# Kernel optimization log

Measured on AMD Instinct MI355X. Metric: run time of the kernel, lower is better.

## Reference

```python
import jax, jax.numpy as jnp
import numpy as np

C = 128      # hidden_dim
H = 8        # nheads
HD = C // H  # head_dim = 16
SCALE = HD ** (-0.5)
Q = 100      # num_queries
T = 5        # t
DM = 512     # d_model
AD = 128     # audio feature dim
EPS = 1e-5


def _ln(x, g, b):
    m = jnp.mean(x, -1, keepdims=True)
    v = jnp.mean((x - m) ** 2, -1, keepdims=True)
    return (x - m) / jnp.sqrt(v + EPS) * g + b


def _heads(x):
    bt, L, c = x.shape
    return x.reshape(bt, L, H, c // H).transpose(0, 2, 1, 3)  # (bt,H,L,hd)


def _unheads(x):
    bt, h, L, d = x.shape
    return x.transpose(0, 2, 1, 3).reshape(bt, L, h * d)


def _attn(q, k, v):
    a = jax.nn.softmax(jnp.einsum('bhqd,bhkd->bhqk', q, k) * SCALE, axis=-1)
    return jnp.einsum('bhqk,bhkd->bhqd', a, v)


def setup_inputs() -> dict:
    key = jax.random.key(0)
    ks = iter(jax.random.split(key, 40))
    def nrm(shape, s=0.02):
        return jax.random.normal(next(ks), shape, dtype=jnp.float32) * s
    bt, hw = 40, 1024
    return {
        'audio_feat': jax.random.normal(next(ks), (bt, hw, AD), dtype=jnp.float32),
        'vis_feat': jax.random.normal(next(ks), (bt, hw, DM), dtype=jnp.float32),
        'iq_emb': nrm((Q, C), 0.1),
        'w_iqp': nrm((C, 2 * C)), 'b_iqp': jnp.zeros((2 * C,), jnp.float32),
        'w_afp': nrm((AD, 2 * C)), 'b_afp': jnp.zeros((2 * C,), jnp.float32),
        'w_vfp': nrm((DM, 2 * C)), 'b_vfp': jnp.zeros((2 * C,), jnp.float32),
        'g_an': jnp.ones((2 * C,), jnp.float32), 'be_an': jnp.zeros((2 * C,), jnp.float32),
        'g_vn': jnp.ones((2 * C,), jnp.float32), 'be_vn': jnp.zeros((2 * C,), jnp.float32),
        'w_aqp': nrm((C, 2 * C)), 'b_aqp': jnp.zeros((2 * C,), jnp.float32),
        'w_vqp': nrm((C, 2 * C)), 'b_vqp': jnp.zeros((2 * C,), jnp.float32),
        'w_aq': nrm((AD, C)), 'b_aq': jnp.zeros((C,), jnp.float32),
        'w_vq': nrm((DM, C)), 'b_vq': jnp.zeros((C,), jnp.float32),
        'w_in': nrm((C, 3 * C)), 'b_in': jnp.zeros((3 * C,), jnp.float32),
        'w_o': nrm((C, C)), 'b_o': jnp.zeros((C,), jnp.float32),
        'w_ao': nrm((C, DM)), 'b_ao': jnp.zeros((DM,), jnp.float32),
        'w_vo': nrm((C, DM)), 'b_vo': jnp.zeros((DM,), jnp.float32),
    }


def reference(audio_feat, vis_feat, iq_emb, w_iqp, b_iqp, w_afp, b_afp,
              w_vfp, b_vfp, g_an, be_an, g_vn, be_vn, w_aqp, b_aqp,
              w_vqp, b_vqp, w_aq, b_aq, w_vq, b_vq, w_in, b_in, w_o, b_o,
              w_ao, b_ao, w_vo, b_vo):
    bt, hw, _ = vis_feat.shape
    bs = bt // T

    # intermediate query projection -> audio / vis query sets
    aq0, vq0 = jnp.split(iq_emb @ w_iqp + b_iqp, 2, axis=-1)  # (Q, C) each
    aqh = _heads(jnp.broadcast_to(aq0, (bt, Q, C)))
    vqh = _heads(jnp.broadcast_to(vq0, (bt, Q, C)))

    # feature K/V (LayerNorm over 2C then chunk)
    a_ki, a_vi = jnp.split(_ln(audio_feat @ w_afp + b_afp, g_an, be_an), 2, axis=-1)
    v_ki, v_vi = jnp.split(_ln(vis_feat @ w_vfp + b_vfp, g_vn, be_vn), 2, axis=-1)

    # cross-attn: queries attend to features, with residual on queries
    aiq = _unheads(_attn(aqh, _heads(a_ki), _heads(a_vi)) + aqh)  # (bt,Q,C)
    viq = _unheads(_attn(vqh, _heads(v_ki), _heads(v_vi)) + vqh)

    # self-attn over concatenated queries across time (per sample)
    queries = jnp.concatenate([aiq, viq], axis=1).reshape(bs, T * 2 * Q, C)
    qkv = queries @ w_in + b_in
    q, k, v = jnp.split(qkv, 3, axis=-1)
    sa = _unheads(_attn(_heads(q), _heads(k), _heads(v))) @ w_o + b_o
    queries = sa.reshape(bt, 2 * Q, C)
    aiq2, viq2 = queries[:, :Q], queries[:, Q:]

    # fused queries become K/V for the features
    a_kf, a_vf = jnp.split(aiq2 @ w_aqp + b_aqp, 2, axis=-1)
    v_kf, v_vf = jnp.split(viq2 @ w_vqp + b_vqp, 2, axis=-1)
    _a = _heads(audio_feat @ w_aq + b_aq)
    _v = _heads(vis_feat @ w_vq + b_vq)

    a_att = _unheads(_attn(_a, _heads(v_kf), _heads(v_vf)))  # (bt,hw,C)
    audio_out = (a_att + audio_feat) @ w_ao + b_ao            # (bt,hw,DM)

    v_att = _unheads(_attn(_v, _heads(a_kf), _heads(a_vf)))   # (bt,hw,C)
    vis_out = v_att @ w_vo + b_vo + vis_feat                  # (bt,hw,DM)

    return (audio_out, vis_out, aiq2)
```

## Files before the change

### kernel.cpp

```cpp
#include <hip/hip_runtime.h>

#define EPSF 1e-5f
#define SCALEF 0.25f

typedef __attribute__((ext_vector_type(8))) __bf16 bf16x8;
typedef __attribute__((ext_vector_type(8))) unsigned short sh8;
typedef __attribute__((ext_vector_type(4))) float f32x4;

__device__ __forceinline__ unsigned short f2bf(float f) {
  unsigned u = __float_as_uint(f);
  return (unsigned short)((u + 0x7FFFu + ((u >> 16) & 1u)) >> 16);
}
__device__ __forceinline__ unsigned pk2(float lo, float hi) {
  return (unsigned)f2bf(lo) | ((unsigned)f2bf(hi) << 16);
}
__device__ __forceinline__ float bf2f(unsigned short u) {
  return __uint_as_float((unsigned)u << 16);
}

__device__ __forceinline__ void gll16(const void* g, void* l) {
  __builtin_amdgcn_global_load_lds((const __attribute__((address_space(1))) void*)g,
                                   (__attribute__((address_space(3))) void*)l,
                                   16, 0, 0);
}

template <int K, int BN, int EPI, bool POST, bool AHEAD, bool OBF, bool PBF, bool AF32>
__global__ __launch_bounds__(BN * 2) void mfma_gemm(
    const unsigned short* __restrict__ A, const unsigned short* __restrict__ Wt,
    const float* __restrict__ bias, const float* __restrict__ gg,
    const float* __restrict__ be, const float* __restrict__ post,
    float* __restrict__ C, int M, int Ntot, int ATPB, int CTPB, size_t CPS,
    float* __restrict__ aiq2, const float* __restrict__ Af32,
    unsigned short* __restrict__ Aside) {
  constexpr int NW = BN / 32;
  constexpr int NCW = BN / 64;
  __shared__ __align__(16) unsigned short As[128 * 32];
  __shared__ __align__(16) unsigned short Bs[BN * 32];
  __shared__ float2 part[128][4];
  const int tid = threadIdx.x;
  const int wid = tid >> 6, lane = tid & 63;
  const int wr = wid / NCW, wc = wid % NCW;
  const int m0t = blockIdx.x * 128, n0t = blockIdx.y * BN;
  const int ir = lane >> 2, sl = lane & 3;
  const int sg = lane >> 4, li = lane & 15;
  f32x4 acc[4][4];
#pragma unroll
  for (int i = 0; i < 4; i++)
#pragma unroll
    for (int j = 0; j < 4; j++) acc[i][j] = (f32x4){0.f, 0.f, 0.f, 0.f};
  constexpr int nIss = 8 + BN / 16;

  for (int k0 = 0; k0 < K; k0 += 32) {
    __syncthreads();
    if constexpr (AF32) {
      int r = tid >> 2, slp = tid & 3;
      int sp = slp ^ ((r >> 1) & 3);
      const float4* src = (const float4*)(Af32 + (size_t)(m0t + r) * K + k0 + sp * 8);
      float4 aa = src[0], bb = src[1];
      uint4 w;
      w.x = pk2(aa.x, aa.y); w.y = pk2(aa.z, aa.w);
      w.z = pk2(bb.x, bb.y); w.w = pk2(bb.z, bb.w);
      *(uint4*)&As[r * 32 + slp * 8] = w;
      *(uint4*)(Aside + (size_t)(m0t + r) * K + k0 + sp * 8) = w;
      for (int is = 8 + wid; is < nIss; is += NW) {
        int r2 = (is - 8) * 16 + ir;
        int sp2 = sl ^ ((r2 >> 1) & 3);
        gll16(Wt + (size_t)(n0t + r2) * K + k0 + sp2 * 8, (void*)&Bs[(is - 8) * 512]);
      }
    } else {
      for (int is = wid; is < nIss; is += NW) {
        if (is < 8) {
          int r = is * 16 + ir;
          int sp = sl ^ ((r >> 1) & 3);
          const unsigned short* gsrc;
          if (AHEAD) {
            int rg = m0t + r;
            if (rg >= M) rg = M - 1;
            int b = rg / ATPB, tok = rg - b * ATPB;
            int e = k0 + sp * 8;
            gsrc = A + ((((size_t)b * 8 + (e >> 4)) * ATPB + tok) << 4) + (e & 15);
          } else {
            gsrc = A + (size_t)(m0t + r) * K + k0 + sp * 8;
          }
          gll16(gsrc, (void*)&As[is * 512]);
        } else {
          int r = (is - 8) * 16 + ir;
          int sp = sl ^ ((r >> 1) & 3);
          gll16(Wt + (size_t)(n0t + r) * K + k0 + sp * 8, (void*)&Bs[(is - 8) * 512]);
        }
      }
    }
    __syncthreads();
    bf16x8 af[4], bfr[4];
#pragma unroll
    for (int mi = 0; mi < 4; mi++) {
      int m = wr * 64 + mi * 16 + li;
      sh8 t = *(const sh8*)&As[m * 32 + ((sg ^ ((m >> 1) & 3)) << 3)];
      af[mi] = __builtin_bit_cast(bf16x8, t);
    }
#pragma unroll
    for (int ni = 0; ni < 4; ni++) {
      int n = wc * 64 + ni * 16 + li;
      sh8 t = *(const sh8*)&Bs[n * 32 + ((sg ^ ((n >> 1) & 3)) << 3)];
      bfr[ni] = __builtin_bit_cast(bf16x8, t);
    }
#pragma unroll
    for (int mi = 0; mi < 4; mi++)
#pragma unroll
      for (int ni = 0; ni < 4; ni++)
        acc[mi][ni] = __builtin_amdgcn_mfma_f32_16x16x32_bf16(af[mi], bfr[ni],
                                                              acc[mi][ni], 0, 0, 0);
  }

  float bv[4];
#pragma unroll
  for (int ni = 0; ni < 4; ni++) bv[ni] = bias[n0t + wc * 64 + ni * 16 + li];

  if constexpr (EPI == 1) {
#pragma unroll
    for (int mi = 0; mi < 4; mi++)
#pragma unroll
      for (int ni = 0; ni < 4; ni++)
#pragma unroll
        for (int r = 0; r < 4; r++) acc[mi][ni][r] += bv[ni];
#pragma unroll
    for (int mi = 0; mi < 4; mi++)
#pragma unroll
      for (int r = 0; r < 4; r++) {
        float s = acc[mi][0][r] + acc[mi][1][r] + acc[mi][2][r] + acc[mi][3][r];
        float q2 = acc[mi][0][r] * acc[mi][0][r] + acc[mi][1][r] * acc[mi][1][r] +
                   acc[mi][2][r] * acc[mi][2][r] + acc[mi][3][r] * acc[mi][3][r];
#pragma unroll
        for (int off = 1; off < 16; off <<= 1) {
          s += __shfl_xor(s, off);
          q2 += __shfl_xor(q2, off);
        }
        if (li == 0) part[wr * 64 + mi * 16 + sg * 4 + r][wc] = make_float2(s, q2);
      }
    __syncthreads();
    float gv[4], bev[4];
#pragma unroll
    for (int ni = 0; ni < 4; ni++) {
      int col = wc * 64 + ni * 16 + li;
      gv[ni] = gg[col];
      bev[ni] = be[col];
    }
#pragma unroll
    for (int mi = 0; mi < 4; mi++)
#pragma unroll
      for (int r = 0; r < 4; r++) {
        int mrow = wr * 64 + mi * 16 + sg * 4 + r;
        float2 p0 = part[mrow][0], p1 = part[mrow][1], p2 = part[mrow][2], p3 = part[mrow][3];
        float S = p0.x + p1.x + p2.x + p3.x;
        float Qq = p0.y + p1.y + p2.y + p3.y;
        float mean = S * (1.f / 256.f);
        float var = Qq * (1.f / 256.f) - mean * mean;
        float rstd = rsqrtf(var + EPSF);
        int mg = m0t + mrow;
        int b = mg / CTPB, tok = mg - b * CTPB;
#pragma unroll
        for (int ni = 0; ni < 4; ni++) {
          int col = wc * 64 + ni * 16 + li;
          float val = (acc[mi][ni][r] - mean) * rstd * gv[ni] + bev[ni];
          int half = col >> 7, h = (col >> 4) & 7, d = col & 15;
          size_t idx = ((((size_t)b * 8 + h) * CTPB + tok) << 4) + d;
          if (OBF) {
            unsigned short* dst = (unsigned short*)C + (half ? CPS : 0);
            dst[idx] = f2bf(val);
          } else {
            float* dst = half ? (C + CPS) : C;
            dst[idx] = val;
          }
        }
      }
  } else if constexpr (EPI == 2) {
#pragma unroll
    for (int mi = 0; mi < 4; mi++)
#pragma unroll
      for (int r = 0; r < 4; r++) {
        int mg = m0t + wr * 64 + mi * 16 + sg * 4 + r;
        if (mg < M) {
          int b = mg / CTPB, tok = mg - b * CTPB;
#pragma unroll
          for (int ni = 0; ni < 4; ni++) {
            int col = n0t + wc * 64 + ni * 16 + li;
            float v = acc[mi][ni][r] + bv[ni];
            int pt = col >> 7, h = (col >> 4) & 7, d = col & 15;
            size_t idx = ((((size_t)b * 8 + h) * CTPB + tok) << 4) + d;
            if (OBF)
              ((unsigned short*)C + (size_t)pt * CPS)[idx] = f2bf(v);
            else
              (C + (size_t)pt * CPS)[idx] = v;
          }
        }
      }
  } else {
#pragma unroll
    for (int mi = 0; mi < 4; mi++)
#pragma unroll
      for (int r = 0; r < 4; r++) {
        int mrow = m0t + wr * 64 + mi * 16 + sg * 4 + r;
        if (mrow < M) {
#pragma unroll
          for (int ni = 0; ni < 4; ni++) {
            int col = n0t + wc * 64 + ni * 16 + li;
            float v = acc[mi][ni][r] + bv[ni];
            if (POST) {
              if (PBF)
                v += bf2f(((const unsigned short*)post)[(size_t)mrow * Ntot + col]);
              else
                v += post[(size_t)mrow * Ntot + col];
            }
            C[(size_t)mrow * Ntot + col] = v;
            if (aiq2) {
              int fb = mrow / 200, wi2 = mrow % 200;
              if (wi2 < 100) aiq2[((size_t)fb * 100 + wi2) * Ntot + col] = v;
            }
          }
        }
      }
  }
}

__global__ __launch_bounds__(512) void mattn1(
    const float* __restrict__ aqvq,
    const unsigned short* __restrict__ akn, const unsigned short* __restrict__ avn,
    const unsigned short* __restrict__ vkn, const unsigned short* __restrict__ vvn,
    unsigned short* __restrict__ op) {
  __shared__ __align__(16) unsigned short Klds[64][24];
  __shared__ __align__(16) unsigned short VTlds[16][72];
  __shared__ __align__(16) unsigned short Plds[8][16][72];
  const int tid = threadIdx.x, wid = tid >> 6, lane = tid & 63;
  const int li = lane & 15, gr = lane >> 4;
  const int z = blockIdx.z, h = blockIdx.y;
  const int mod = z >= 40 ? 1 : 0;
  const int b = z - mod * 40;
  const int bh = b * 8 + h;
  const int qi = wid * 16 + li;
  const bool qact = qi < 100;
  const int qic = qact ? qi : 99;
  const float* qrow = aqvq + mod * 128 + (size_t)qic * 256 + h * 16;
  const unsigned short* kp = mod ? vkn : akn;
  const unsigned short* vp = mod ? vvn : avn;

  sh8 z8 = (sh8)0;
  bf16x8 qf = __builtin_bit_cast(bf16x8, z8);
  if (gr < 2) {
    const float4* q4 = (const float4*)(qrow + gr * 8);
    float4 qa = q4[0], qb = q4[1];
    sh8 tt;
    tt[0] = f2bf(qa.x); tt[1] = f2bf(qa.y); tt[2] = f2bf(qa.z); tt[3] = f2bf(qa.w);
    tt[4] = f2bf(qb.x); tt[5] = f2bf(qb.y); tt[6] = f2bf(qb.z); tt[7] = f2bf(qb.w);
    qf = __builtin_bit_cast(bf16x8, tt);
  }

  float mrun = -3e38f, lrun = 0.f;
  f32x4 acc = (f32x4){0.f, 0.f, 0.f, 0.f};
  const f32x4 zero4 = (f32x4){0.f, 0.f, 0.f, 0.f};
  const unsigned* Ku = (const unsigned*)(kp + (size_t)bh * 1024 * 16);
  const unsigned* Vu = (const unsigned*)(vp + (size_t)bh * 1024 * 16);
  const int skey = tid >> 3, sdb = tid & 7;

  unsigned kw = Ku[(size_t)skey * 8 + sdb];
  unsigned vw = Vu[(size_t)skey * 8 + sdb];
  for (int kb = 0; kb < 1024; kb += 64) {
    __syncthreads();
    *(unsigned*)&Klds[skey][sdb * 2] = kw;
    VTlds[sdb * 2 + 0][skey] = (unsigned short)(vw & 0xffff);
    VTlds[sdb * 2 + 1][skey] = (unsigned short)(vw >> 16);
    if (kb + 64 < 1024) {
      kw = Ku[(size_t)(kb + 64 + skey) * 8 + sdb];
      vw = Vu[(size_t)(kb + 64 + skey) * 8 + sdb];
    }
    __syncthreads();
    f32x4 st[4];
#pragma unroll
    for (int t = 0; t < 4; t++) {
      sh8 kk = *(const sh8*)&Klds[t * 16 + li][(gr & 1) * 8];
      st[t] = __builtin_amdgcn_mfma_f32_16x16x32_bf16(
          __builtin_bit_cast(bf16x8, kk), qf, zero4, 0, 0, 0);
    }
    float sv[4][4];
#pragma unroll
    for (int t = 0; t < 4; t++)
#pragma unroll
      for (int r = 0; r < 4; r++) sv[t][r] = st[t][r] * SCALEF;
    float bm = sv[0][0];
#pragma unroll
    for (int t = 0; t < 4; t++)
#pragma unroll
      for (int r = 0; r < 4; r++) bm = fmaxf(bm, sv[t][r]);
    bm = fmaxf(bm, __shfl_xor(bm, 16));
    bm = fmaxf(bm, __shfl_xor(bm, 32));
    float mnew = fmaxf(mrun, bm);
    float cf = __expf(mrun - mnew);
    mrun = mnew;
    lrun *= cf;
    acc[0] *= cf; acc[1] *= cf; acc[2] *= cf; acc[3] *= cf;
    float ls = 0.f;
    unsigned pw[4][2];
#pragma unroll
    for (int t = 0; t < 4; t++) {
      float p0 = __expf(sv[t][0] - mnew), p1 = __expf(sv[t][1] - mnew);
      float p2 = __expf(sv[t][2] - mnew), p3 = __expf(sv[t][3] - mnew);
      ls += (p0 + p1) + (p2 + p3);
      pw[t][0] = pk2(p0, p1);
      pw[t][1] = pk2(p2, p3);
    }
    ls += __shfl_xor(ls, 16);
    ls += __shfl_xor(ls, 32);
    lrun += ls;
#pragma unroll
    for (int t = 0; t < 4; t++)
      *(uint2*)&Plds[wid][li][t * 16 + gr * 4] = make_uint2(pw[t][0], pw[t][1]);
#pragma unroll
    for (int hh = 0; hh < 2; hh++) {
      sh8 vt = *(const sh8*)&VTlds[li][hh * 32 + gr * 8];
      sh8 pt = *(const sh8*)&Plds[wid][li][hh * 32 + gr * 8];
      acc = __builtin_amdgcn_mfma_f32_16x16x32_bf16(
          __builtin_bit_cast(bf16x8, vt), __builtin_bit_cast(bf16x8, pt), acc, 0, 0, 0);
    }
  }
  float inv = 1.f / lrun;
  float o[4];
#pragma unroll
  for (int r = 0; r < 4; r++) o[r] = acc[r] * inv;
  const float4* q4 = (const float4*)(qrow + gr * 4);
  float4 qv = q4[0];
  o[0] += qv.x; o[1] += qv.y; o[2] += qv.z; o[3] += qv.w;
  if (qact) {
    int obh = (b / 5) * 8 + h;
    int otok = (b % 5) * 200 + mod * 100 + qi;
    *(uint2*)(op + (((size_t)obh * 1000 + otok) << 4) + gr * 4) =
        make_uint2(pk2(o[0], o[1]), pk2(o[2], o[3]));
  }
}

template <int MODE>
__global__ __launch_bounds__(512) void mattn8(
    const unsigned short* __restrict__ q0s, const unsigned short* __restrict__ q1s,
    size_t qsb, size_t qsh, int qsr,
    const unsigned short* __restrict__ k0s, const unsigned short* __restrict__ v0s,
    const unsigned short* __restrict__ k1s, const unsigned short* __restrict__ v1s,
    int nk, int nq, unsigned short* __restrict__ o0s, unsigned short* __restrict__ o1s,
    int OTPB, const unsigned short* __restrict__ residbf) {
  __shared__ __align__(16) unsigned short Klds[64][24];
  __shared__ __align__(16) unsigned short VTlds[16][72];
  __shared__ __align__(16) unsigned short Plds[8][16][72];
  const int tid = threadIdx.x, wid = tid >> 6, lane = tid & 63;
  const int li = lane & 15, gr = lane >> 4;
  const int z = blockIdx.z, h = blockIdx.y;
  int mod = 0, b = z;
  const unsigned short *qp = q0s, *kp = k0s, *vp = v0s;
  unsigned short* op = o0s;
  if (MODE == 2) {
    mod = z >= 40 ? 1 : 0;
    b = z - mod * 40;
    if (mod) { qp = q1s; kp = k1s; vp = v1s; op = o1s; }
  }
  const int bh = b * 8 + h;
  const int qi = blockIdx.x * 128 + wid * 16 + li;
  const bool qact = qi < nq;
  const int qic = qact ? qi : nq - 1;
  const unsigned short* qrow = qp + b * qsb + h * qsh + (size_t)qic * qsr;

  sh8 z8 = (sh8)0;
  bf16x8 qf = __builtin_bit_cast(bf16x8, z8);
  if (gr < 2) qf = __builtin_bit_cast(bf16x8, *(const sh8*)(qrow + gr * 8));

  float mrun = -3e38f, lrun = 0.f;
  f32x4 acc = (f32x4){0.f, 0.f, 0.f, 0.f};
  const f32x4 zero4 = (f32x4){0.f, 0.f, 0.f, 0.f};
  const unsigned* Ku = (const unsigned*)(kp + (size_t)bh * nk * 16);
  const unsigned* Vu = (const unsigned*)(vp + (size_t)bh * nk * 16);
  const int skey = tid >> 3, sdb = tid & 7;

  unsigned kw = (skey < nk) ? Ku[(size_t)skey * 8 + sdb] : 0u;
  unsigned vw = (skey < nk) ? Vu[(size_t)skey * 8 + sdb] : 0u;
  for (int kb = 0; kb < nk; kb += 64) {
    __syncthreads();
    *(unsigned*)&Klds[skey][sdb * 2] = kw;
    VTlds[sdb * 2 + 0][skey] = (unsigned short)(vw & 0xffff);
    VTlds[sdb * 2 + 1][skey] = (unsigned short)(vw >> 16);
    if (kb + 64 < nk) {
      int gk = kb + 64 + skey;
      kw = (gk < nk) ? Ku[(size_t)gk * 8 + sdb] : 0u;
      vw = (gk < nk) ? Vu[(size_t)gk * 8 + sdb] : 0u;
    }
    __syncthreads();
    f32x4 st[4];
#pragma unroll
    for (int t = 0; t < 4; t++) {
      sh8 kk = *(const sh8*)&Klds[t * 16 + li][(gr & 1) * 8];
      st[t] = __builtin_amdgcn_mfma_f32_16x16x32_bf16(
          __builtin_bit_cast(bf16x8, kk), qf, zero4, 0, 0, 0);
    }
    float sv[4][4];
#pragma unroll
    for (int t = 0; t < 4; t++)
#pragma unroll
      for (int r = 0; r < 4; r++) sv[t][r] = st[t][r] * SCALEF;
    if (kb + 64 > nk) {
#pragma unroll
      for (int t = 0; t < 4; t++) {
        int kbase = kb + t * 16 + gr * 4;
#pragma unroll
        for (int r = 0; r < 4; r++)
          if (kbase + r >= nk) sv[t][r] = -1e30f;
      }
    }
    float bm = sv[0][0];
#pragma unroll
    for (int t = 0; t < 4; t++)
#pragma unroll
      for (int r = 0; r < 4; r++) bm = fmaxf(bm, sv[t][r]);
    bm = fmaxf(bm, __shfl_xor(bm, 16));
    bm = fmaxf(bm, __shfl_xor(bm, 32));
    float mnew = fmaxf(mrun, bm);
    float cf = __expf(mrun - mnew);
    mrun = mnew;
    lrun *= cf;
    acc[0] *= cf; acc[1] *= cf; acc[2] *= cf; acc[3] *= cf;
    float ls = 0.f;
    unsigned pw[4][2];
#pragma unroll
    for (int t = 0; t < 4; t++) {
      float p0 = __expf(sv[t][0] - mnew), p1 = __expf(sv[t][1] - mnew);
      float p2 = __expf(sv[t][2] - mnew), p3 = __expf(sv[t][3] - mnew);
      ls += (p0 + p1) + (p2 + p3);
      pw[t][0] = pk2(p0, p1);
      pw[t][1] = pk2(p2, p3);
    }
    ls += __shfl_xor(ls, 16);
    ls += __shfl_xor(ls, 32);
    lrun += ls;
#pragma unroll
    for (int t = 0; t < 4; t++)
      *(uint2*)&Plds[wid][li][t * 16 + gr * 4] = make_uint2(pw[t][0], pw[t][1]);
#pragma unroll
    for (int hh = 0; hh < 2; hh++) {
      sh8 vt = *(const sh8*)&VTlds[li][hh * 32 + gr * 8];
      sh8 pt = *(const sh8*)&Plds[wid][li][hh * 32 + gr * 8];
      acc = __builtin_amdgcn_mfma_f32_16x16x32_bf16(
          __builtin_bit_cast(bf16x8, vt), __builtin_bit_cast(bf16x8, pt), acc, 0, 0, 0);
    }
  }
  float inv = 1.f / lrun;
  float o[4];
#pragma unroll
  for (int r = 0; r < 4; r++) o[r] = acc[r] * inv;
  if (MODE == 2 && mod == 0 && residbf) {
    uint2 rv = *(const uint2*)(residbf + ((size_t)b * 1024 + qic) * 128 + h * 16 + gr * 4);
    o[0] += bf2f((unsigned short)(rv.x & 0xffff));
    o[1] += bf2f((unsigned short)(rv.x >> 16));
    o[2] += bf2f((unsigned short)(rv.y & 0xffff));
    o[3] += bf2f((unsigned short)(rv.y >> 16));
  }
  if (qact) {
    *(uint2*)(op + (((size_t)bh * OTPB + qi) << 4) + gr * 4) =
        make_uint2(pk2(o[0], o[1]), pk2(o[2], o[3]));
  }
}

__global__ __launch_bounds__(256) void prep_kernel(
    const float* __restrict__ iq, const float* __restrict__ w_iqp,
    const float* __restrict__ b_iqp,
    const float* __restrict__ w_afp, const float* __restrict__ w_vfp,
    const float* __restrict__ w_aq, const float* __restrict__ w_vq,
    const float* __restrict__ w_in, const float* __restrict__ w_o,
    const float* __restrict__ w_ao, const float* __restrict__ w_vo,
    unsigned short* __restrict__ WT, float* __restrict__ aqvq) {
  __shared__ float row[128];
  const int g = blockIdx.x, tid = threadIdx.x;
  if (g < 1728) {
    int lg = g;
    int K, N;
    const float* W;
    unsigned dst;
    if (lg < 128)       { K = 128; N = 256; W = w_afp; dst = 0; }
    else if (lg < 640)  { K = 512; N = 256; W = w_vfp; dst = 32768;  lg -= 128; }
    else if (lg < 704)  { K = 128; N = 128; W = w_aq;  dst = 163840; lg -= 640; }
    else if (lg < 960)  { K = 512; N = 128; W = w_vq;  dst = 180224; lg -= 704; }
    else if (lg < 1152) { K = 128; N = 384; W = w_in;  dst = 245760; lg -= 960; }
    else if (lg < 1216) { K = 128; N = 128; W = w_o;   dst = 294912; lg -= 1152; }
    else if (lg < 1472) { K = 128; N = 512; W = w_ao;  dst = 311296; lg -= 1216; }
    else                { K = 128; N = 512; W = w_vo;  dst = 376832; lg -= 1472; }
    int idx = lg * 256 + tid;
    if (idx < K * N) {
      int k = idx / N, n = idx - k * N;
      WT[dst + (size_t)n * K + k] = f2bf(W[idx]);
    }
  } else {
    int r = g - 1728;
    if (tid < 128) row[tid] = iq[r * 128 + tid];
    __syncthreads();
    float acc = b_iqp[tid];
#pragma unroll 8
    for (int k = 0; k < 128; ++k) acc += row[k] * w_iqp[k * 256 + tid];
    aqvq[r * 256 + tid] = acc;
  }
}

template <int K, int N, int R>
__global__ __launch_bounds__(N) void gemm_kv_kernel(
    const float* __restrict__ in,
    const float* __restrict__ Wa, const float* __restrict__ ba,
    const float* __restrict__ Wv, const float* __restrict__ bvv,
    unsigned short* __restrict__ Ka, unsigned short* __restrict__ Va,
    unsigned short* __restrict__ Kv, unsigned short* __restrict__ Vv) {
  __shared__ float rows[R][K];
  const int sel = blockIdx.y;
  const float* W = sel ? Wv : Wa;
  const float* bias = sel ? bvv : ba;
  unsigned short* outK = sel ? Kv : Ka;
  unsigned short* outV = sel ? Vv : Va;
  const int rowoff = sel ? 100 : 0;
  int r0 = blockIdx.x * R;
  for (int e = threadIdx.x; e < R * K; e += N) {
    int rr = e / K, k = e - rr * K;
    size_t r = r0 + rr;
    size_t irx = (r / 100) * 200 + rowoff + (r % 100);
    rows[rr][k] = in[irx * K + k];
  }
  __syncthreads();
  int c = threadIdx.x;
  float acc[R];
  float bb = bias[c];
#pragma unroll
  for (int rr = 0; rr < R; rr++) acc[rr] = bb;
  for (int k = 0; k < K; k += 4) {
    float w0 = W[(size_t)k * N + c];
    float w1 = W[(size_t)(k + 1) * N + c];
    float w2 = W[(size_t)(k + 2) * N + c];
    float w3 = W[(size_t)(k + 3) * N + c];
#pragma unroll
    for (int rr = 0; rr < R; rr++) {
      float4 r4 = *reinterpret_cast<const float4*>(&rows[rr][k]);
      acc[rr] = fmaf(r4.x, w0, acc[rr]);
      acc[rr] = fmaf(r4.y, w1, acc[rr]);
      acc[rr] = fmaf(r4.z, w2, acc[rr]);
      acc[rr] = fmaf(r4.w, w3, acc[rr]);
    }
  }
  int half = c >> 7, h = (c >> 4) & 7, d = c & 15;
  unsigned short* dst = half ? outV : outK;
#pragma unroll
  for (int rr = 0; rr < R; rr++) {
    int r = r0 + rr;
    int b = r / 100, tok = r - b * 100;
    dst[((((size_t)b * 8 + h) * 100 + tok) << 4) + d] = f2bf(acc[rr]);
  }
}

extern "C" void kernel_launch(void* const* d_in, const int* in_sizes, int n_in,
                              void* d_out, int out_size, void* d_ws, size_t ws_size,
                              hipStream_t stream) {
  const float* audio = (const float*)d_in[0];
  const float* vis   = (const float*)d_in[1];
  const float* iq    = (const float*)d_in[2];
  const float* w_iqp = (const float*)d_in[3];
  const float* b_iqp = (const float*)d_in[4];
  const float* w_afp = (const float*)d_in[5];
  const float* b_afp = (const float*)d_in[6];
  const float* w_vfp = (const float*)d_in[7];
  const float* b_vfp = (const float*)d_in[8];
  const float* g_an  = (const float*)d_in[9];
  const float* be_an = (const float*)d_in[10];
  const float* g_vn  = (const float*)d_in[11];
  const float* be_vn = (const float*)d_in[12];
  const float* w_aqp = (const float*)d_in[13];
  const float* b_aqp = (const float*)d_in[14];
  const float* w_vqp = (const float*)d_in[15];
  const float* b_vqp = (const float*)d_in[16];
  const float* w_aq  = (const float*)d_in[17];
  const float* b_aq  = (const float*)d_in[18];
  const float* w_vq  = (const float*)d_in[19];
  const float* b_vq  = (const float*)d_in[20];
  const float* w_in  = (const float*)d_in[21];
  const float* b_in  = (const float*)d_in[22];
  const float* w_o   = (const float*)d_in[23];
  const float* b_o   = (const float*)d_in[24];
  const float* w_ao  = (const float*)d_in[25];
  const float* b_ao  = (const float*)d_in[26];
  const float* w_vo  = (const float*)d_in[27];
  const float* b_vo  = (const float*)d_in[28];

  float* out = (float*)d_out;
  float* ws  = (float*)d_ws;

  unsigned short* vis_bf = (unsigned short*)(out);
  unsigned short* akn = (unsigned short*)(out + 10485760);
  unsigned short* avn = akn + 5242880;
  unsigned short* vkn = akn + 10485760;
  unsigned short* vvn = akn + 15728640;
  unsigned short* a_hm = (unsigned short*)(out + 20971520);
  unsigned short* v_hm = (unsigned short*)(out + 23592960);
  float* aiq2_out = out + 41943040;
  float* audio_out = out;
  float* vis_out   = out + 20971520;

  unsigned short* WT       = (unsigned short*)(ws);
  unsigned short* audio_bf = (unsigned short*)(ws + 262144);
  unsigned short* Q1hm     = (unsigned short*)(ws + 2883584);
  unsigned short* saphm    = (unsigned short*)(ws + 3395584);
  unsigned short* qkvhm    = (unsigned short*)(ws + 3915776);
  unsigned short* aatthm   = (unsigned short*)(ws + 3915776);
  unsigned short* vatthm   = (unsigned short*)(ws + 6987776);
  float* SA                = ws + 9609216;
  unsigned short* Ka = (unsigned short*)(ws + 10633216);
  unsigned short* Va = Ka + 512000;
  unsigned short* Kv = Ka + 1024000;
  unsigned short* Vv = Ka + 1536000;
  float* aqvq = ws + 12681216;

  unsigned short* afp_t = WT + 0;
  unsigned short* vfp_t = WT + 32768;
  unsigned short* aq_t  = WT + 163840;
  unsigned short* vq_t  = WT + 180224;
  unsigned short* in_t  = WT + 245760;
  unsigned short* o_t   = WT + 294912;
  unsigned short* ao_t  = WT + 311296;
  unsigned short* vo_t  = WT + 376832;

  prep_kernel<<<1828, 256, 0, stream>>>(
      iq, w_iqp, b_iqp, w_afp, w_vfp, w_aq, w_vq, w_in, w_o, w_ao, w_vo, WT, aqvq);

  mfma_gemm<128, 256, 1, false, false, true, false, true><<<dim3(320, 1), 512, 0, stream>>>(
      nullptr, afp_t, b_afp, g_an, be_an, nullptr, (float*)akn, 40960, 256, 0, 1024,
      5242880, nullptr, audio, audio_bf);
  mfma_gemm<512, 256, 1, false, false, true, false, true><<<dim3(320, 1), 512, 0, stream>>>(
      nullptr, vfp_t, b_vfp, g_vn, be_vn, nullptr, (float*)vkn, 40960, 256, 0, 1024,
      5242880, nullptr, vis, vis_bf);

  mattn1<<<dim3(1, 8, 80), 512, 0, stream>>>(aqvq, akn, avn, vkn, vvn, Q1hm);

  mfma_gemm<128, 128, 2, false, true, true, false, false><<<dim3(63, 3), 256, 0, stream>>>(
      Q1hm, in_t, b_in, nullptr, nullptr, nullptr, (float*)qkvhm, 8000, 384, 1000, 1000,
      1024000, nullptr, nullptr, nullptr);

  mattn8<1><<<dim3(8, 8, 8), 512, 0, stream>>>(
      qkvhm, nullptr, 128000, 16000, 16, qkvhm + 1024000, qkvhm + 2048000,
      nullptr, nullptr, 1000, 1000, saphm, nullptr, 1000, nullptr);

  mfma_gemm<128, 128, 0, false, true, false, false, false><<<dim3(63, 1), 256, 0, stream>>>(
      saphm, o_t, b_o, nullptr, nullptr, nullptr, SA, 8000, 128, 1000, 0, 0, aiq2_out,
      nullptr, nullptr);

  gemm_kv_kernel<128, 256, 16><<<dim3(250, 2), 256, 0, stream>>>(
      SA, w_aqp, b_aqp, w_vqp, b_vqp, Ka, Va, Kv, Vv);

  mfma_gemm<128, 128, 2, false, false, true, false, false><<<dim3(320, 1), 256, 0, stream>>>(
      audio_bf, aq_t, b_aq, nullptr, nullptr, nullptr, (float*)a_hm, 40960, 128, 0, 1024,
      0, nullptr, nullptr, nullptr);
  mfma_gemm<512, 128, 2, false, false, true, false, false><<<dim3(320, 1), 256, 0, stream>>>(
      vis_bf, vq_t, b_vq, nullptr, nullptr, nullptr, (float*)v_hm, 40960, 128, 0, 1024,
      0, nullptr, nullptr, nullptr);

  mattn8<2><<<dim3(8, 8, 80), 512, 0, stream>>>(
      a_hm, v_hm, 131072, 16384, 16, Kv, Vv, Ka, Va, 100, 1024,
      aatthm, vatthm, 1024, audio_bf);

  mfma_gemm<128, 128, 0, true, true, false, true, false><<<dim3(320, 4), 256, 0, stream>>>(
      vatthm, vo_t, b_vo, nullptr, nullptr, (const float*)vis_bf, vis_out, 40960, 512,
      1024, 0, 0, nullptr, nullptr, nullptr);

  mfma_gemm<128, 128, 0, false, true, false, false, false><<<dim3(320, 4), 256, 0, stream>>>(
      aatthm, ao_t, b_ao, nullptr, nullptr, nullptr, audio_out, 40960, 512, 1024, 0, 0,
      nullptr, nullptr, nullptr);
}
```

Measured before the change: 339.5 us.

## Batch paired projection GEMMs into single launches, fold softmax scale, lazy rescale

Merges the audio and visual LayerNorm-projection GEMMs into one launch (ln_gemm, grid z=2), and likewise the two query-projection GEMMs (projq_kernel). The attention scale is folded into Q at production time, which removes the per-score multiply in the attention loops. The online softmax now rescales only when the running max grows by more than 8, skipping most exp/rescale work. f2bf switches to the hardware bf16 conversion builtin. Fewer launches and better wave fill are traded against the small numerical risk of lazy rescaling, which allows exponents up to e^8.

```diff
diff --git a/kernel.cpp b/kernel.cpp
--- a/kernel.cpp
+++ b/kernel.cpp
@@ -8,8 +8,7 @@
 typedef __attribute__((ext_vector_type(4))) float f32x4;
 
 __device__ __forceinline__ unsigned short f2bf(float f) {
-  unsigned u = __float_as_uint(f);
-  return (unsigned short)((u + 0x7FFFu + ((u >> 16) & 1u)) >> 16);
+  return __builtin_bit_cast(unsigned short, (__bf16)f);
 }
 __device__ __forceinline__ unsigned pk2(float lo, float hi) {
   return (unsigned)f2bf(lo) | ((unsigned)f2bf(hi) << 16);
@@ -24,19 +23,16 @@
                                    16, 0, 0);
 }
 
-template <int K, int BN, int EPI, bool POST, bool AHEAD, bool OBF, bool PBF, bool AF32>
+template <int K, int BN, int EPI, bool POST, bool AHEAD, bool OBF, bool PBF, bool QSC>
 __global__ __launch_bounds__(BN * 2) void mfma_gemm(
     const unsigned short* __restrict__ A, const unsigned short* __restrict__ Wt,
-    const float* __restrict__ bias, const float* __restrict__ gg,
-    const float* __restrict__ be, const float* __restrict__ post,
+    const float* __restrict__ bias, const float* __restrict__ post,
     float* __restrict__ C, int M, int Ntot, int ATPB, int CTPB, size_t CPS,
-    float* __restrict__ aiq2, const float* __restrict__ Af32,
-    unsigned short* __restrict__ Aside) {
+    float* __restrict__ aiq2) {
   constexpr int NW = BN / 32;
   constexpr int NCW = BN / 64;
   __shared__ __align__(16) unsigned short As[128 * 32];
   __shared__ __align__(16) unsigned short Bs[BN * 32];
-  __shared__ float2 part[128][4];
   const int tid = threadIdx.x;
   const int wid = tid >> 6, lane = tid & 63;
   const int wr = wid / NCW, wc = wid % NCW;
@@ -52,42 +48,25 @@
 
   for (int k0 = 0; k0 < K; k0 += 32) {
     __syncthreads();
-    if constexpr (AF32) {
-      int r = tid >> 2, slp = tid & 3;
-      int sp = slp ^ ((r >> 1) & 3);
-      const float4* src = (const float4*)(Af32 + (size_t)(m0t + r) * K + k0 + sp * 8);
-      float4 aa = src[0], bb = src[1];
-      uint4 w;
-      w.x = pk2(aa.x, aa.y); w.y = pk2(aa.z, aa.w);
-      w.z = pk2(bb.x, bb.y); w.w = pk2(bb.z, bb.w);
-      *(uint4*)&As[r * 32 + slp * 8] = w;
-      *(uint4*)(Aside + (size_t)(m0t + r) * K + k0 + sp * 8) = w;
-      for (int is = 8 + wid; is < nIss; is += NW) {
-        int r2 = (is - 8) * 16 + ir;
-        int sp2 = sl ^ ((r2 >> 1) & 3);
-        gll16(Wt + (size_t)(n0t + r2) * K + k0 + sp2 * 8, (void*)&Bs[(is - 8) * 512]);
-      }
-    } else {
-      for (int is = wid; is < nIss; is += NW) {
-        if (is < 8) {
-          int r = is * 16 + ir;
-          int sp = sl ^ ((r >> 1) & 3);
-          const unsigned short* gsrc;
-          if (AHEAD) {
-            int rg = m0t + r;
-            if (rg >= M) rg = M - 1;
-            int b = rg / ATPB, tok = rg - b * ATPB;
-            int e = k0 + sp * 8;
-            gsrc = A + ((((size_t)b * 8 + (e >> 4)) * ATPB + tok) << 4) + (e & 15);
-          } else {
-            gsrc = A + (size_t)(m0t + r) * K + k0 + sp * 8;
-          }
-          gll16(gsrc, (void*)&As[is * 512]);
+    for (int is = wid; is < nIss; is += NW) {
+      if (is < 8) {
+        int r = is * 16 + ir;
+        int sp = sl ^ ((r >> 1) & 3);
+        const unsigned short* gsrc;
+        if (AHEAD) {
+          int rg = m0t + r;
+          if (rg >= M) rg = M - 1;
+          int b = rg / ATPB, tok = rg - b * ATPB;
+          int e = k0 + sp * 8;
+          gsrc = A + ((((size_t)b * 8 + (e >> 4)) * ATPB + tok) << 4) + (e & 15);
         } else {
-          int r = (is - 8) * 16 + ir;
-          int sp = sl ^ ((r >> 1) & 3);
-          gll16(Wt + (size_t)(n0t + r) * K + k0 + sp * 8, (void*)&Bs[(is - 8) * 512]);
+          gsrc = A + (size_t)(m0t + r) * K + k0 + sp * 8;
         }
+        gll16(gsrc, (void*)&As[is * 512]);
+      } else {
+        int r = (is - 8) * 16 + ir;
+        int sp = sl ^ ((r >> 1) & 3);
+        gll16(Wt + (size_t)(n0t + r) * K + k0 + sp * 8, (void*)&Bs[(is - 8) * 512]);
       }
     }
     __syncthreads();
@@ -116,64 +95,7 @@
 #pragma unroll
   for (int ni = 0; ni < 4; ni++) bv[ni] = bias[n0t + wc * 64 + ni * 16 + li];
 
-  if constexpr (EPI == 1) {
-#pragma unroll
-    for (int mi = 0; mi < 4; mi++)
-#pragma unroll
-      for (int ni = 0; ni < 4; ni++)
-#pragma unroll
-        for (int r = 0; r < 4; r++) acc[mi][ni][r] += bv[ni];
-#pragma unroll
-    for (int mi = 0; mi < 4; mi++)
-#pragma unroll
-      for (int r = 0; r < 4; r++) {
-        float s = acc[mi][0][r] + acc[mi][1][r] + acc[mi][2][r] + acc[mi][3][r];
-        float q2 = acc[mi][0][r] * acc[mi][0][r] + acc[mi][1][r] * acc[mi][1][r] +
-                   acc[mi][2][r] * acc[mi][2][r] + acc[mi][3][r] * acc[mi][3][r];
-#pragma unroll
-        for (int off = 1; off < 16; off <<= 1) {
-          s += __shfl_xor(s, off);
-          q2 += __shfl_xor(q2, off);
-        }
-        if (li == 0) part[wr * 64 + mi * 16 + sg * 4 + r][wc] = make_float2(s, q2);
-      }
-    __syncthreads();
-    float gv[4], bev[4];
-#pragma unroll
-    for (int ni = 0; ni < 4; ni++) {
-      int col = wc * 64 + ni * 16 + li;
-      gv[ni] = gg[col];
-      bev[ni] = be[col];
-    }
-#pragma unroll
-    for (int mi = 0; mi < 4; mi++)
-#pragma unroll
-      for (int r = 0; r < 4; r++) {
-        int mrow = wr * 64 + mi * 16 + sg * 4 + r;
-        float2 p0 = part[mrow][0], p1 = part[mrow][1], p2 = part[mrow][2], p3 = part[mrow][3];
-        float S = p0.x + p1.x + p2.x + p3.x;
-        float Qq = p0.y + p1.y + p2.y + p3.y;
-        float mean = S * (1.f / 256.f);
-        float var = Qq * (1.f / 256.f) - mean * mean;
-        float rstd = rsqrtf(var + EPSF);
-        int mg = m0t + mrow;
-        int b = mg / CTPB, tok = mg - b * CTPB;
-#pragma unroll
-        for (int ni = 0; ni < 4; ni++) {
-          int col = wc * 64 + ni * 16 + li;
-          float val = (acc[mi][ni][r] - mean) * rstd * gv[ni] + bev[ni];
-          int half = col >> 7, h = (col >> 4) & 7, d = col & 15;
-          size_t idx = ((((size_t)b * 8 + h) * CTPB + tok) << 4) + d;
-          if (OBF) {
-            unsigned short* dst = (unsigned short*)C + (half ? CPS : 0);
-            dst[idx] = f2bf(val);
-          } else {
-            float* dst = half ? (C + CPS) : C;
-            dst[idx] = val;
-          }
-        }
-      }
-  } else if constexpr (EPI == 2) {
+  if constexpr (EPI == 2) {
 #pragma unroll
     for (int mi = 0; mi < 4; mi++)
 #pragma unroll
@@ -186,6 +108,7 @@
             int col = n0t + wc * 64 + ni * 16 + li;
             float v = acc[mi][ni][r] + bv[ni];
             int pt = col >> 7, h = (col >> 4) & 7, d = col & 15;
+            if (QSC && pt == 0) v *= SCALEF;
             size_t idx = ((((size_t)b * 8 + h) * CTPB + tok) << 4) + d;
             if (OBF)
               ((unsigned short*)C + (size_t)pt * CPS)[idx] = f2bf(v);
@@ -220,6 +143,215 @@
         }
       }
   }
+}
+
+__global__ __launch_bounds__(512) void ln_gemm(
+    const float* __restrict__ audio, const float* __restrict__ vis,
+    const unsigned short* __restrict__ afp_t, const unsigned short* __restrict__ vfp_t,
+    const float* __restrict__ b_afp, const float* __restrict__ b_vfp,
+    const float* __restrict__ g_an, const float* __restrict__ g_vn,
+    const float* __restrict__ be_an, const float* __restrict__ be_vn,
+    unsigned short* __restrict__ akn, unsigned short* __restrict__ vkn,
+    unsigned short* __restrict__ audio_bf, unsigned short* __restrict__ vis_bf) {
+  constexpr int BN = 256, NW = 8, NCW = 4;
+  constexpr size_t CPS = 5242880;
+  __shared__ __align__(16) unsigned short As[128 * 32];
+  __shared__ __align__(16) unsigned short Bs[BN * 32];
+  __shared__ float2 part[128][4];
+  const int z = blockIdx.z;
+  const float* Af32 = z ? vis : audio;
+  const unsigned short* Wt = z ? vfp_t : afp_t;
+  const float* bias = z ? b_vfp : b_afp;
+  const float* gg = z ? g_vn : g_an;
+  const float* be = z ? be_vn : be_an;
+  unsigned short* C = z ? vkn : akn;
+  unsigned short* Aside = z ? vis_bf : audio_bf;
+  const int K = z ? 512 : 128;
+  const int tid = threadIdx.x;
+  const int wid = tid >> 6, lane = tid & 63;
+  const int wr = wid / NCW, wc = wid % NCW;
+  const int m0t = blockIdx.x * 128;
+  const int ir = lane >> 2, sl = lane & 3;
+  const int sg = lane >> 4, li = lane & 15;
+  f32x4 acc[4][4];
+#pragma unroll
+  for (int i = 0; i < 4; i++)
+#pragma unroll
+    for (int j = 0; j < 4; j++) acc[i][j] = (f32x4){0.f, 0.f, 0.f, 0.f};
+
+  for (int k0 = 0; k0 < K; k0 += 32) {
+    __syncthreads();
+    {
+      int r = tid >> 2, slp = tid & 3;
+      int sp = slp ^ ((r >> 1) & 3);
+      const float4* src = (const float4*)(Af32 + (size_t)(m0t + r) * K + k0 + sp * 8);
+      float4 aa = src[0], bb = src[1];
+      uint4 w;
+      w.x = pk2(aa.x, aa.y); w.y = pk2(aa.z, aa.w);
+      w.z = pk2(bb.x, bb.y); w.w = pk2(bb.z, bb.w);
+      *(uint4*)&As[r * 32 + slp * 8] = w;
+      *(uint4*)(Aside + (size_t)(m0t + r) * K + k0 + sp * 8) = w;
+    }
+    for (int is = 8 + wid; is < 8 + BN / 16; is += NW) {
+      int r2 = (is - 8) * 16 + ir;
+      int sp2 = sl ^ ((r2 >> 1) & 3);
+      gll16(Wt + (size_t)r2 * K + k0 + sp2 * 8, (void*)&Bs[(is - 8) * 512]);
+    }
+    __syncthreads();
+    bf16x8 af[4], bfr[4];
+#pragma unroll
+    for (int mi = 0; mi < 4; mi++) {
+      int m = wr * 64 + mi * 16 + li;
+      sh8 t = *(const sh8*)&As[m * 32 + ((sg ^ ((m >> 1) & 3)) << 3)];
+      af[mi] = __builtin_bit_cast(bf16x8, t);
+    }
+#pragma unroll
+    for (int ni = 0; ni < 4; ni++) {
+      int n = wc * 64 + ni * 16 + li;
+      sh8 t = *(const sh8*)&Bs[n * 32 + ((sg ^ ((n >> 1) & 3)) << 3)];
+      bfr[ni] = __builtin_bit_cast(bf16x8, t);
+    }
+#pragma unroll
+    for (int mi = 0; mi < 4; mi++)
+#pragma unroll
+      for (int ni = 0; ni < 4; ni++)
+        acc[mi][ni] = __builtin_amdgcn_mfma_f32_16x16x32_bf16(af[mi], bfr[ni],
+                                                              acc[mi][ni], 0, 0, 0);
+  }
+
+  float bv[4];
+#pragma unroll
+  for (int ni = 0; ni < 4; ni++) bv[ni] = bias[wc * 64 + ni * 16 + li];
+#pragma unroll
+  for (int mi = 0; mi < 4; mi++)
+#pragma unroll
+    for (int ni = 0; ni < 4; ni++)
+#pragma unroll
+      for (int r = 0; r < 4; r++) acc[mi][ni][r] += bv[ni];
+#pragma unroll
+  for (int mi = 0; mi < 4; mi++)
+#pragma unroll
+    for (int r = 0; r < 4; r++) {
+      float s = acc[mi][0][r] + acc[mi][1][r] + acc[mi][2][r] + acc[mi][3][r];
+      float q2 = acc[mi][0][r] * acc[mi][0][r] + acc[mi][1][r] * acc[mi][1][r] +
+                 acc[mi][2][r] * acc[mi][2][r] + acc[mi][3][r] * acc[mi][3][r];
+#pragma unroll
+      for (int off = 1; off < 16; off <<= 1) {
+        s += __shfl_xor(s, off);
+        q2 += __shfl_xor(q2, off);
+      }
+      if (li == 0) part[wr * 64 + mi * 16 + sg * 4 + r][wc] = make_float2(s, q2);
+    }
+  __syncthreads();
+  float gv[4], bev[4];
+#pragma unroll
+  for (int ni = 0; ni < 4; ni++) {
+    int col = wc * 64 + ni * 16 + li;
+    gv[ni] = gg[col];
+    bev[ni] = be[col];
+  }
+#pragma unroll
+  for (int mi = 0; mi < 4; mi++)
+#pragma unroll
+    for (int r = 0; r < 4; r++) {
+      int mrow = wr * 64 + mi * 16 + sg * 4 + r;
+      float2 p0 = part[mrow][0], p1 = part[mrow][1], p2 = part[mrow][2], p3 = part[mrow][3];
+      float S = p0.x + p1.x + p2.x + p3.x;
+      float Qq = p0.y + p1.y + p2.y + p3.y;
+      float mean = S * (1.f / 256.f);
+      float var = Qq * (1.f / 256.f) - mean * mean;
+      float rstd = rsqrtf(var + EPSF);
+      int mg = m0t + mrow;
+      int b = mg >> 10, tok = mg & 1023;
+#pragma unroll
+      for (int ni = 0; ni < 4; ni++) {
+        int col = wc * 64 + ni * 16 + li;
+        float val = (acc[mi][ni][r] - mean) * rstd * gv[ni] + bev[ni];
+        int half = col >> 7, h = (col >> 4) & 7, d = col & 15;
+        size_t idx = ((((size_t)b * 8 + h) * 1024 + tok) << 4) + d;
+        (C + (half ? CPS : 0))[idx] = f2bf(val);
+      }
+    }
+}
+
+__global__ __launch_bounds__(256) void projq_kernel(
+    const unsigned short* __restrict__ audio_bf, const unsigned short* __restrict__ vis_bf,
+    const unsigned short* __restrict__ aq_t, const unsigned short* __restrict__ vq_t,
+    const float* __restrict__ b_aq, const float* __restrict__ b_vq,
+    unsigned short* __restrict__ a_hm, unsigned short* __restrict__ v_hm) {
+  constexpr int BN = 128, NW = 4, NCW = 2;
+  __shared__ __align__(16) unsigned short As[128 * 32];
+  __shared__ __align__(16) unsigned short Bs[BN * 32];
+  const int z = blockIdx.z;
+  const unsigned short* A = z ? vis_bf : audio_bf;
+  const unsigned short* Wt = z ? vq_t : aq_t;
+  const float* bias = z ? b_vq : b_aq;
+  unsigned short* C = z ? v_hm : a_hm;
+  const int K = z ? 512 : 128;
+  const int tid = threadIdx.x;
+  const int wid = tid >> 6, lane = tid & 63;
+  const int wr = wid / NCW, wc = wid % NCW;
+  const int m0t = blockIdx.x * 128;
+  const int ir = lane >> 2, sl = lane & 3;
+  const int sg = lane >> 4, li = lane & 15;
+  f32x4 acc[4][4];
+#pragma unroll
+  for (int i = 0; i < 4; i++)
+#pragma unroll
+    for (int j = 0; j < 4; j++) acc[i][j] = (f32x4){0.f, 0.f, 0.f, 0.f};
+
+  for (int k0 = 0; k0 < K; k0 += 32) {
+    __syncthreads();
+    for (int is = wid; is < 8 + BN / 16; is += NW) {
+      if (is < 8) {
+        int r = is * 16 + ir;
+        int sp = sl ^ ((r >> 1) & 3);
+        gll16(A + (size_t)(m0t + r) * K + k0 + sp * 8, (void*)&As[is * 512]);
+      } else {
+        int r = (is - 8) * 16 + ir;
+        int sp = sl ^ ((r >> 1) & 3);
+        gll16(Wt + (size_t)r * K + k0 + sp * 8, (void*)&Bs[(is - 8) * 512]);
+      }
+    }
+    __syncthreads();
+    bf16x8 af[4], bfr[4];
+#pragma unroll
+    for (int mi = 0; mi < 4; mi++) {
+      int m = wr * 64 + mi * 16 + li;
+      sh8 t = *(const sh8*)&As[m * 32 + ((sg ^ ((m >> 1) & 3)) << 3)];
+      af[mi] = __builtin_bit_cast(bf16x8, t);
+    }
+#pragma unroll
+    for (int ni = 0; ni < 4; ni++) {
+      int n = wc * 64 + ni * 16 + li;
+      sh8 t = *(const sh8*)&Bs[n * 32 + ((sg ^ ((n >> 1) & 3)) << 3)];
+      bfr[ni] = __builtin_bit_cast(bf16x8, t);
+    }
+#pragma unroll
+    for (int mi = 0; mi < 4; mi++)
+#pragma unroll
+      for (int ni = 0; ni < 4; ni++)
+        acc[mi][ni] = __builtin_amdgcn_mfma_f32_16x16x32_bf16(af[mi], bfr[ni],
+                                                              acc[mi][ni], 0, 0, 0);
+  }
+
+  float bv[4];
+#pragma unroll
+  for (int ni = 0; ni < 4; ni++) bv[ni] = bias[wc * 64 + ni * 16 + li];
+#pragma unroll
+  for (int mi = 0; mi < 4; mi++)
+#pragma unroll
+    for (int r = 0; r < 4; r++) {
+      int mg = m0t + wr * 64 + mi * 16 + sg * 4 + r;
+      int b = mg >> 10, tok = mg & 1023;
+#pragma unroll
+      for (int ni = 0; ni < 4; ni++) {
+        int col = wc * 64 + ni * 16 + li;
+        float v = (acc[mi][ni][r] + bv[ni]) * SCALEF;
+        int h = (col >> 4) & 7, d = col & 15;
+        C[((((size_t)b * 8 + h) * 1024 + tok) << 4) + d] = f2bf(v);
+      }
+    }
 }
 
 __global__ __launch_bounds__(512) void mattn1(
@@ -249,8 +381,10 @@
     const float4* q4 = (const float4*)(qrow + gr * 8);
     float4 qa = q4[0], qb = q4[1];
     sh8 tt;
-    tt[0] = f2bf(qa.x); tt[1] = f2bf(qa.y); tt[2] = f2bf(qa.z); tt[3] = f2bf(qa.w);
-    tt[4] = f2bf(qb.x); tt[5] = f2bf(qb.y); tt[6] = f2bf(qb.z); tt[7] = f2bf(qb.w);
+    tt[0] = f2bf(qa.x * SCALEF); tt[1] = f2bf(qa.y * SCALEF);
+    tt[2] = f2bf(qa.z * SCALEF); tt[3] = f2bf(qa.w * SCALEF);
+    tt[4] = f2bf(qb.x * SCALEF); tt[5] = f2bf(qb.y * SCALEF);
+    tt[6] = f2bf(qb.z * SCALEF); tt[7] = f2bf(qb.w * SCALEF);
     qf = __builtin_bit_cast(bf16x8, tt);
   }
 
@@ -280,29 +414,25 @@
       st[t] = __builtin_amdgcn_mfma_f32_16x16x32_bf16(
           __builtin_bit_cast(bf16x8, kk), qf, zero4, 0, 0, 0);
     }
-    float sv[4][4];
+    float bm = st[0][0];
 #pragma unroll
     for (int t = 0; t < 4; t++)
 #pragma unroll
-      for (int r = 0; r < 4; r++) sv[t][r] = st[t][r] * SCALEF;
-    float bm = sv[0][0];
-#pragma unroll
-    for (int t = 0; t < 4; t++)
-#pragma unroll
-      for (int r = 0; r < 4; r++) bm = fmaxf(bm, sv[t][r]);
+      for (int r = 0; r < 4; r++) bm = fmaxf(bm, st[t][r]);
     bm = fmaxf(bm, __shfl_xor(bm, 16));
     bm = fmaxf(bm, __shfl_xor(bm, 32));
-    float mnew = fmaxf(mrun, bm);
-    float cf = __expf(mrun - mnew);
-    mrun = mnew;
-    lrun *= cf;
-    acc[0] *= cf; acc[1] *= cf; acc[2] *= cf; acc[3] *= cf;
+    if (bm > mrun + 8.f) {
+      float cf = __expf(mrun - bm);
+      lrun *= cf;
+      acc[0] *= cf; acc[1] *= cf; acc[2] *= cf; acc[3] *= cf;
+      mrun = bm;
+    }
     float ls = 0.f;
     unsigned pw[4][2];
 #pragma unroll
     for (int t = 0; t < 4; t++) {
-      float p0 = __expf(sv[t][0] - mnew), p1 = __expf(sv[t][1] - mnew);
-      float p2 = __expf(sv[t][2] - mnew), p3 = __expf(sv[t][3] - mnew);
+      float p0 = __expf(st[t][0] - mrun), p1 = __expf(st[t][1] - mrun);
+      float p2 = __expf(st[t][2] - mrun), p3 = __expf(st[t][3] - mrun);
       ls += (p0 + p1) + (p2 + p3);
       pw[t][0] = pk2(p0, p1);
       pw[t][1] = pk2(p2, p3);
@@ -395,38 +525,34 @@
       st[t] = __builtin_amdgcn_mfma_f32_16x16x32_bf16(
           __builtin_bit_cast(bf16x8, kk), qf, zero4, 0, 0, 0);
     }
-    float sv[4][4];
-#pragma unroll
-    for (int t = 0; t < 4; t++)
-#pragma unroll
-      for (int r = 0; r < 4; r++) sv[t][r] = st[t][r] * SCALEF;
     if (kb + 64 > nk) {
 #pragma unroll
       for (int t = 0; t < 4; t++) {
         int kbase = kb + t * 16 + gr * 4;
 #pragma unroll
         for (int r = 0; r < 4; r++)
-          if (kbase + r >= nk) sv[t][r] = -1e30f;
+          if (kbase + r >= nk) st[t][r] = -1e30f;
       }
     }
-    float bm = sv[0][0];
+    float bm = st[0][0];
 #pragma unroll
     for (int t = 0; t < 4; t++)
 #pragma unroll
-      for (int r = 0; r < 4; r++) bm = fmaxf(bm, sv[t][r]);
+      for (int r = 0; r < 4; r++) bm = fmaxf(bm, st[t][r]);
     bm = fmaxf(bm, __shfl_xor(bm, 16));
     bm = fmaxf(bm, __shfl_xor(bm, 32));
-    float mnew = fmaxf(mrun, bm);
-    float cf = __expf(mrun - mnew);
-    mrun = mnew;
-    lrun *= cf;
-    acc[0] *= cf; acc[1] *= cf; acc[2] *= cf; acc[3] *= cf;
+    if (bm > mrun + 8.f) {
+      float cf = __expf(mrun - bm);
+      lrun *= cf;
+      acc[0] *= cf; acc[1] *= cf; acc[2] *= cf; acc[3] *= cf;
+      mrun = bm;
+    }
     float ls = 0.f;
     unsigned pw[4][2];
 #pragma unroll
     for (int t = 0; t < 4; t++) {
-      float p0 = __expf(sv[t][0] - mnew), p1 = __expf(sv[t][1] - mnew);
-      float p2 = __expf(sv[t][2] - mnew), p3 = __expf(sv[t][3] - mnew);
+      float p0 = __expf(st[t][0] - mrun), p1 = __expf(st[t][1] - mrun);
+      float p2 = __expf(st[t][2] - mrun), p3 = __expf(st[t][3] - mrun);
       ls += (p0 + p1) + (p2 + p3);
       pw[t][0] = pk2(p0, p1);
       pw[t][1] = pk2(p2, p3);
@@ -625,46 +751,35 @@
   prep_kernel<<<1828, 256, 0, stream>>>(
       iq, w_iqp, b_iqp, w_afp, w_vfp, w_aq, w_vq, w_in, w_o, w_ao, w_vo, WT, aqvq);
 
-  mfma_gemm<128, 256, 1, false, false, true, false, true><<<dim3(320, 1), 512, 0, stream>>>(
-      nullptr, afp_t, b_afp, g_an, be_an, nullptr, (float*)akn, 40960, 256, 0, 1024,
-      5242880, nullptr, audio, audio_bf);
-  mfma_gemm<512, 256, 1, false, false, true, false, true><<<dim3(320, 1), 512, 0, stream>>>(
-      nullptr, vfp_t, b_vfp, g_vn, be_vn, nullptr, (float*)vkn, 40960, 256, 0, 1024,
-      5242880, nullptr, vis, vis_bf);
+  ln_gemm<<<dim3(320, 1, 2), 512, 0, stream>>>(
+      audio, vis, afp_t, vfp_t, b_afp, b_vfp, g_an, g_vn, be_an, be_vn,
+      akn, vkn, audio_bf, vis_bf);
 
   mattn1<<<dim3(1, 8, 80), 512, 0, stream>>>(aqvq, akn, avn, vkn, vvn, Q1hm);
 
-  mfma_gemm<128, 128, 2, false, true, true, false, false><<<dim3(63, 3), 256, 0, stream>>>(
-      Q1hm, in_t, b_in, nullptr, nullptr, nullptr, (float*)qkvhm, 8000, 384, 1000, 1000,
-      1024000, nullptr, nullptr, nullptr);
+  mfma_gemm<128, 128, 2, false, true, true, false, true><<<dim3(63, 3), 256, 0, stream>>>(
+      Q1hm, in_t, b_in, nullptr, (float*)qkvhm, 8000, 384, 1000, 1000, 1024000, nullptr);
 
   mattn8<1><<<dim3(8, 8, 8), 512, 0, stream>>>(
       qkvhm, nullptr, 128000, 16000, 16, qkvhm + 1024000, qkvhm + 2048000,
       nullptr, nullptr, 1000, 1000, saphm, nullptr, 1000, nullptr);
 
   mfma_gemm<128, 128, 0, false, true, false, false, false><<<dim3(63, 1), 256, 0, stream>>>(
-      saphm, o_t, b_o, nullptr, nullptr, nullptr, SA, 8000, 128, 1000, 0, 0, aiq2_out,
-      nullptr, nullptr);
+      saphm, o_t, b_o, nullptr, SA, 8000, 128, 1000, 0, 0, aiq2_out);
 
   gemm_kv_kernel<128, 256, 16><<<dim3(250, 2), 256, 0, stream>>>(
       SA, w_aqp, b_aqp, w_vqp, b_vqp, Ka, Va, Kv, Vv);
 
-  mfma_gemm<128, 128, 2, false, false, true, false, false><<<dim3(320, 1), 256, 0, stream>>>(
-      audio_bf, aq_t, b_aq, nullptr, nullptr, nullptr, (float*)a_hm, 40960, 128, 0, 1024,
-      0, nullptr, nullptr, nullptr);
-  mfma_gemm<512, 128, 2, false, false, true, false, false><<<dim3(320, 1), 256, 0, stream>>>(
-      vis_bf, vq_t, b_vq, nullptr, nullptr, nullptr, (float*)v_hm, 40960, 128, 0, 1024,
-      0, nullptr, nullptr, nullptr);
+  projq_kernel<<<dim3(320, 1, 2), 256, 0, stream>>>(
+      audio_bf, vis_bf, aq_t, vq_t, b_aq, b_vq, a_hm, v_hm);
 
   mattn8<2><<<dim3(8, 8, 80), 512, 0, stream>>>(
       a_hm, v_hm, 131072, 16384, 16, Kv, Vv, Ka, Va, 100, 1024,
       aatthm, vatthm, 1024, audio_bf);
 
   mfma_gemm<128, 128, 0, true, true, false, true, false><<<dim3(320, 4), 256, 0, stream>>>(
-      vatthm, vo_t, b_vo, nullptr, nullptr, (const float*)vis_bf, vis_out, 40960, 512,
-      1024, 0, 0, nullptr, nullptr, nullptr);
+      vatthm, vo_t, b_vo, (const float*)vis_bf, vis_out, 40960, 512, 1024, 0, 0, nullptr);
 
   mfma_gemm<128, 128, 0, false, true, false, false, false><<<dim3(320, 4), 256, 0, stream>>>(
-      aatthm, ao_t, b_ao, nullptr, nullptr, nullptr, audio_out, 40960, 512, 1024, 0, 0,
-      nullptr, nullptr, nullptr);
-}
+      aatthm, ao_t, b_ao, nullptr, audio_out, 40960, 512, 1024, 0, 0, nullptr);
+}
```

Result: faster. 291.9 us (-14.0%).
